# Performance work log

Measured on AMD Instinct MI355X. Metric: run time of the kernel, lower is better.

Reference implementation:

```python
import jax, jax.numpy as jnp
import numpy as np

N_NODES = 50000
N_EDGES = 800000
IN_F = 64
HID_F = 64
OUT_F = 12


def setup_inputs() -> dict:
    key = jax.random.key(0)
    ks = jax.random.split(key, 8)
    x = jax.random.normal(ks[0], (N_NODES, IN_F), dtype=jnp.float32)
    edge_index = jax.random.randint(ks[1], (2, N_EDGES), 0, N_NODES, dtype=jnp.int64)
    edge_attr = jax.random.uniform(ks[2], (N_EDGES, 1), dtype=jnp.float32)
    # Glorot-ish scaled weights
    W1 = jax.random.normal(ks[3], (IN_F, HID_F), dtype=jnp.float32) / np.sqrt(IN_F)
    b1 = jnp.zeros((HID_F,), dtype=jnp.float32)
    W2 = jax.random.normal(ks[4], (HID_F, HID_F), dtype=jnp.float32) / np.sqrt(HID_F)
    b2 = jnp.zeros((HID_F,), dtype=jnp.float32)
    Wfc = jax.random.normal(ks[5], (HID_F, OUT_F), dtype=jnp.float32) / np.sqrt(HID_F)
    bfc = jnp.zeros((OUT_F,), dtype=jnp.float32)
    return {"x": x, "edge_index": edge_index, "edge_attr": edge_attr,
            "W1": W1, "b1": b1, "W2": W2, "b2": b2, "Wfc": Wfc, "bfc": bfc}


def _gcn_conv(h, src, dst, ew, W, b, n_nodes):
    """PyG GCNConv: linear -> add self-loops (weight 1) -> sym-normalized scatter-add -> +bias."""
    hl = h @ W  # [N, F_out]
    loop = jnp.arange(n_nodes, dtype=src.dtype)
    s = jnp.concatenate([src, loop])
    d = jnp.concatenate([dst, loop])
    w = jnp.concatenate([ew, jnp.ones((n_nodes,), dtype=hl.dtype)])
    deg = jax.ops.segment_sum(w, d, num_segments=n_nodes)
    dinv = jnp.where(deg > 0, jax.lax.rsqrt(jnp.maximum(deg, 1e-30)), 0.0)
    norm = dinv[s] * w * dinv[d]  # per-edge coefficient
    out = jax.ops.segment_sum(norm[:, None] * hl[s], d, num_segments=n_nodes)
    return out + b


def reference(x, edge_index, edge_attr, W1, b1, W2, b2, Wfc, bfc):
    src, dst = edge_index[0], edge_index[1]
    ew = edge_attr.squeeze(-1)
    n = x.shape[0]
    h = jax.nn.relu(_gcn_conv(x, src, dst, ew, W1, b1, n))
    h = jax.nn.relu(_gcn_conv(h, src, dst, ew, W2, b2, n))
    return h @ Wfc + bfc
```

## Files before the change

kernel.cpp:

```cpp
#include <hip/hip_runtime.h>
#include <hip/hip_bf16.h>
#include <hip/hip_fp16.h>


#define N_FEAT   64
#define OUT_F    12
#define NTHREADS 256
#define MAXDEG   52
#define AGG_BLOCKS 1792
#define CNT_SHIFT 25
#define SUM_MASK  0x1FFFFFFu
#define FIXS     524288.0f
#define FIXINV   (1.0f / 524288.0f)

struct Params {
    const float* x; const int* idx; const float* ew;
    const float* W1; const float* b1; const float* W2; const float* b2;
    const float* Wfc; const float* bfc;
    float* out;
    int n_nodes, n_edges;
    unsigned int* deg32;
    float* dinv;
    unsigned int* ell;
    __hip_bfloat16* xbf;
    __hip_bfloat16* h1bf;
};

__device__ __forceinline__ float unpack_w(unsigned int e) {
    return __half2float(__ushort_as_half((unsigned short)(e & 0xffffu)));
}

__device__ __forceinline__ void lds_fence() {
    asm volatile("s_waitcnt lgkmcnt(0)" ::: "memory");
}

__device__ __forceinline__ float ell_gather(const __hip_bfloat16* __restrict__ hl,
                                            const unsigned int* __restrict__ row,
                                            int cnt, int lane, float acc) {
    const int nq = cnt >> 2;
    if (nq > 0) {
        uint4 a = *(const uint4*)(row);
        float va0 = __bfloat162float(hl[(a.x >> 16) * 64 + lane]);
        float va1 = __bfloat162float(hl[(a.y >> 16) * 64 + lane]);
        float va2 = __bfloat162float(hl[(a.z >> 16) * 64 + lane]);
        float va3 = __bfloat162float(hl[(a.w >> 16) * 64 + lane]);
        uint4 b = (nq > 1) ? *(const uint4*)(row + 4) : a;
        for (int q = 1; q < nq; q++) {
            uint4 c = (q + 1 < nq) ? *(const uint4*)(row + 4 * (q + 1)) : b;
            float vb0 = __bfloat162float(hl[(b.x >> 16) * 64 + lane]);
            float vb1 = __bfloat162float(hl[(b.y >> 16) * 64 + lane]);
            float vb2 = __bfloat162float(hl[(b.z >> 16) * 64 + lane]);
            float vb3 = __bfloat162float(hl[(b.w >> 16) * 64 + lane]);
            acc += unpack_w(a.x) * va0;
            acc += unpack_w(a.y) * va1;
            acc += unpack_w(a.z) * va2;
            acc += unpack_w(a.w) * va3;
            a = b; va0 = vb0; va1 = vb1; va2 = vb2; va3 = vb3;
            b = c;
        }
        acc += unpack_w(a.x) * va0;
        acc += unpack_w(a.y) * va1;
        acc += unpack_w(a.z) * va2;
        acc += unpack_w(a.w) * va3;
    }
    for (int k = nq << 2; k < cnt; k++) {
        unsigned int e = row[k];
        acc += unpack_w(e) * __bfloat162float(hl[(e >> 16) * 64 + lane]);
    }
    return acc;
}


__global__ void kf_count(Params p) {
    int e2 = blockIdx.x * NTHREADS + threadIdx.x;
    int nE2 = p.n_edges >> 1;
    if (e2 < nE2) {
        int2   s2 = ((const int2*)p.idx)[e2];
        int2   d2 = ((const int2*)(p.idx + p.n_edges))[e2];
        float2 w2 = ((const float2*)p.ew)[e2];
        unsigned int o0 =
            atomicAdd(&p.deg32[d2.x], (1u << CNT_SHIFT) | (unsigned int)(w2.x * FIXS));
        unsigned int o1 =
            atomicAdd(&p.deg32[d2.y], (1u << CNT_SHIFT) | (unsigned int)(w2.y * FIXS));
        int sl0 = (int)(o0 >> CNT_SHIFT);
        int sl1 = (int)(o1 >> CNT_SHIFT);
        if (sl0 < MAXDEG)
            p.ell[d2.x * MAXDEG + sl0] = ((unsigned int)s2.x << 16) |
                                         (unsigned int)__half_as_ushort(__float2half(w2.x));
        if (sl1 < MAXDEG)
            p.ell[d2.y * MAXDEG + sl1] = ((unsigned int)s2.y << 16) |
                                         (unsigned int)__half_as_ushort(__float2half(w2.y));
    }
    if (e2 == 0 && (p.n_edges & 1)) {
        int e = p.n_edges - 1;
        int s = p.idx[e], d = p.idx[p.n_edges + e];
        float w = p.ew[e];
        unsigned int o =
            atomicAdd(&p.deg32[d], (1u << CNT_SHIFT) | (unsigned int)(w * FIXS));
        int sl = (int)(o >> CNT_SHIFT);
        if (sl < MAXDEG)
            p.ell[d * MAXDEG + sl] =
                ((unsigned int)s << 16) | (unsigned int)__half_as_ushort(__float2half(w));
    }
}

__global__ void kf_scalex(Params p) {
    int t = threadIdx.x, b = blockIdx.x, nb = gridDim.x;
    int lane = t & 63;
    int wid  = t >> 6;
    for (int node = b * 4 + wid; node < p.n_nodes; node += nb * 4) {
        unsigned int dv = p.deg32[node];
        float di = rsqrtf((float)(dv & SUM_MASK) * FIXINV + 1.0f);
        float xv = p.x[node * 64 + lane];
        p.xbf[node * 64 + lane] = __float2bfloat16(di * xv);
        if (lane == 0) p.dinv[node] = di;
    }
}

__global__ void kf_agg1g1(Params p) {
    __shared__ float Ws[64 * 64];
    __shared__ float hs[4][64];
    int t = threadIdx.x, b = blockIdx.x, nb = gridDim.x;
    {
        const float4* W4 = (const float4*)p.W1;
        float4* Ws4 = (float4*)Ws;
        for (int i = t; i < 1024; i += NTHREADS) Ws4[i] = W4[i];
    }
    __syncthreads();
    int lane = t & 63;
    int wid  = t >> 6;
    float bv = p.b1[lane];
    float* hrow = hs[wid];
    for (int node = b * 4 + wid; node < p.n_nodes; node += nb * 4) {
        float di = p.dinv[node];
        int cnt = (int)(p.deg32[node] >> CNT_SHIFT);
        cnt = (cnt > MAXDEG) ? MAXDEG : cnt;
        float acc = __bfloat162float(p.xbf[node * 64 + lane]);
        acc = ell_gather(p.xbf, p.ell + (long long)node * MAXDEG, cnt, lane, acc);
        hrow[lane] = di * acc;
        lds_fence();
        float o = 0.f;
#pragma unroll
        for (int k4 = 0; k4 < 16; k4++) {
            float4 hv = *(const float4*)&hrow[k4 * 4];
            int kb = k4 << 2;
            o += hv.x * Ws[(kb + 0) * 64 + lane];
            o += hv.y * Ws[(kb + 1) * 64 + lane];
            o += hv.z * Ws[(kb + 2) * 64 + lane];
            o += hv.w * Ws[(kb + 3) * 64 + lane];
        }
        float h1 = fmaxf(o + bv, 0.0f);
        p.h1bf[node * 64 + lane] = __float2bfloat16(di * h1);
        lds_fence();
    }
}

__global__ void kf_agg2fc(Params p) {
    __shared__ float Ws[64 * 64];
    __shared__ float Wf[64 * OUT_F];
    __shared__ float bf[OUT_F];
    __shared__ float hs[4][64];
    int t = threadIdx.x, b = blockIdx.x, nb = gridDim.x;
    {
        const float4* W4 = (const float4*)p.W2;
        float4* Ws4 = (float4*)Ws;
        for (int i = t; i < 1024; i += NTHREADS) Ws4[i] = W4[i];
    }
    for (int i = t; i < 64 * OUT_F; i += NTHREADS) Wf[i] = p.Wfc[i];
    if (t < OUT_F) bf[t] = p.bfc[t];
    __syncthreads();
    int lane = t & 63;
    int wid  = t >> 6;
    float bv = p.b2[lane];
    float* hrow = hs[wid];
    for (int node = b * 4 + wid; node < p.n_nodes; node += nb * 4) {
        float di  = p.dinv[node];
        int   cnt = (int)(p.deg32[node] >> CNT_SHIFT);
        cnt = (cnt > MAXDEG) ? MAXDEG : cnt;
        float acc = __bfloat162float(p.h1bf[node * 64 + lane]);
        acc = ell_gather(p.h1bf, p.ell + (long long)node * MAXDEG, cnt, lane, acc);
        hrow[lane] = di * acc;
        lds_fence();
        float o = 0.f;
#pragma unroll
        for (int k4 = 0; k4 < 16; k4++) {
            float4 hv = *(const float4*)&hrow[k4 * 4];
            int kb = k4 << 2;
            o += hv.x * Ws[(kb + 0) * 64 + lane];
            o += hv.y * Ws[(kb + 1) * 64 + lane];
            o += hv.z * Ws[(kb + 2) * 64 + lane];
            o += hv.w * Ws[(kb + 3) * 64 + lane];
        }
        float h2 = fmaxf(o + bv, 0.0f);
        lds_fence();
        hrow[lane] = h2;
        lds_fence();
        if (lane < OUT_F) {
            float o2 = bf[lane];
#pragma unroll
            for (int k4 = 0; k4 < 16; k4++) {
                float4 hq = *(const float4*)&hrow[k4 * 4];
                int kb = k4 << 2;
                o2 += hq.x * Wf[(kb + 0) * OUT_F + lane];
                o2 += hq.y * Wf[(kb + 1) * OUT_F + lane];
                o2 += hq.z * Wf[(kb + 2) * OUT_F + lane];
                o2 += hq.w * Wf[(kb + 3) * OUT_F + lane];
            }
            p.out[node * OUT_F + lane] = o2;
        }
        lds_fence();
    }
}

extern "C" void kernel_launch(void* const* d_in, const int* in_sizes, int n_in,
                              void* d_out, int out_size, void* d_ws, size_t ws_size,
                              hipStream_t stream) {
    Params p;
    p.x   = (const float*)d_in[0];
    p.idx = (const int*)d_in[1];
    p.ew  = (const float*)d_in[2];
    p.W1  = (const float*)d_in[3];
    p.b1  = (const float*)d_in[4];
    p.W2  = (const float*)d_in[5];
    p.b2  = (const float*)d_in[6];
    p.Wfc = (const float*)d_in[7];
    p.bfc = (const float*)d_in[8];
    p.out = (float*)d_out;
    p.n_nodes = in_sizes[0] / N_FEAT;
    p.n_edges = in_sizes[2];

    float* ws = (float*)d_ws;
    p.deg32 = (unsigned int*)ws;
    p.dinv  = ws + 100032;
    p.ell   = (unsigned int*)(ws + 150048);
    p.xbf   = (__hip_bfloat16*)(ws + 2750048);
    p.h1bf  = (__hip_bfloat16*)(ws + 4350048);

    int gE2 = (p.n_edges / 2 + NTHREADS - 1) / NTHREADS;

    (void)hipMemsetAsync(ws, 0, 50016u * 4u, stream);
    kf_count <<<gE2,        NTHREADS, 0, stream>>>(p);
    kf_scalex<<<AGG_BLOCKS, NTHREADS, 0, stream>>>(p);
    kf_agg1g1<<<AGG_BLOCKS, NTHREADS, 0, stream>>>(p);
    kf_agg2fc<<<AGG_BLOCKS, NTHREADS, 0, stream>>>(p);
}
```

Before: 213.2 us.

## Prefetch next node's metadata and use wave shuffles instead of LDS rows

Both aggregation kernels now software-pipeline the node loop. The next node's degree word, dinv, self feature and first ELL quad are loaded before the current node's gather runs, which hides the latency of those dependent loads. The per-wave LDS staging row and its waitcnt fences are replaced by __shfl broadcasts for the 64x64 and 64x12 matvecs, and the FC stage now runs on all lanes with clamped indices. The aggregation grid also grows from 1792 to 2048 blocks. The cost is higher register pressure from the prefetched state, and the shuffles go through LDS hardware (ds_bpermute) anyway.

After: 431.3 us. 2.02x slower.

```diff
diff --git a/kernel.cpp b/kernel.cpp
--- a/kernel.cpp
+++ b/kernel.cpp
@@ -7,7 +7,7 @@
 #define OUT_F    12
 #define NTHREADS 256
 #define MAXDEG   52
-#define AGG_BLOCKS 1792
+#define AGG_BLOCKS 2048
 #define CNT_SHIFT 25
 #define SUM_MASK  0x1FFFFFFu
 #define FIXS     524288.0f
@@ -30,16 +30,11 @@
     return __half2float(__ushort_as_half((unsigned short)(e & 0xffffu)));
 }
 
-__device__ __forceinline__ void lds_fence() {
-    asm volatile("s_waitcnt lgkmcnt(0)" ::: "memory");
-}
-
-__device__ __forceinline__ float ell_gather(const __hip_bfloat16* __restrict__ hl,
-                                            const unsigned int* __restrict__ row,
-                                            int cnt, int lane, float acc) {
+__device__ __forceinline__ float ell_gather_pre(const __hip_bfloat16* __restrict__ hl,
+                                                const unsigned int* __restrict__ row,
+                                                int cnt, int lane, float acc, uint4 a) {
     const int nq = cnt >> 2;
     if (nq > 0) {
-        uint4 a = *(const uint4*)(row);
         float va0 = __bfloat162float(hl[(a.x >> 16) * 64 + lane]);
         float va1 = __bfloat162float(hl[(a.y >> 16) * 64 + lane]);
         float va2 = __bfloat162float(hl[(a.z >> 16) * 64 + lane]);
@@ -119,7 +114,6 @@
 
 __global__ void kf_agg1g1(Params p) {
     __shared__ float Ws[64 * 64];
-    __shared__ float hs[4][64];
     int t = threadIdx.x, b = blockIdx.x, nb = gridDim.x;
     {
         const float4* W4 = (const float4*)p.W1;
@@ -130,36 +124,52 @@
     int lane = t & 63;
     int wid  = t >> 6;
     float bv = p.b1[lane];
-    float* hrow = hs[wid];
-    for (int node = b * 4 + wid; node < p.n_nodes; node += nb * 4) {
-        float di = p.dinv[node];
-        int cnt = (int)(p.deg32[node] >> CNT_SHIFT);
+    const int stride = nb * 4;
+    int node = b * 4 + wid;
+    if (node >= p.n_nodes) return;
+    unsigned int dv = p.deg32[node];
+    float di = p.dinv[node];
+    float self = __bfloat162float(p.xbf[node * 64 + lane]);
+    const unsigned int* rowp = p.ell + (long long)node * MAXDEG;
+    uint4 q0 = *(const uint4*)rowp;
+    for (;;) {
+        int nnode = node + stride;
+        bool have_next = (nnode < p.n_nodes);
+        unsigned int ndv = 0; float ndi = 0.f, nself = 0.f;
+        const unsigned int* nrowp = rowp; uint4 nq0 = q0;
+        if (have_next) {
+            ndv   = p.deg32[nnode];
+            ndi   = p.dinv[nnode];
+            nself = __bfloat162float(p.xbf[nnode * 64 + lane]);
+            nrowp = p.ell + (long long)nnode * MAXDEG;
+            nq0   = *(const uint4*)nrowp;
+        }
+        int cnt = (int)(dv >> CNT_SHIFT);
         cnt = (cnt > MAXDEG) ? MAXDEG : cnt;
-        float acc = __bfloat162float(p.xbf[node * 64 + lane]);
-        acc = ell_gather(p.xbf, p.ell + (long long)node * MAXDEG, cnt, lane, acc);
-        hrow[lane] = di * acc;
-        lds_fence();
+        float g = di * ell_gather_pre(p.xbf, rowp, cnt, lane, self, q0);
         float o = 0.f;
 #pragma unroll
-        for (int k4 = 0; k4 < 16; k4++) {
-            float4 hv = *(const float4*)&hrow[k4 * 4];
-            int kb = k4 << 2;
-            o += hv.x * Ws[(kb + 0) * 64 + lane];
-            o += hv.y * Ws[(kb + 1) * 64 + lane];
-            o += hv.z * Ws[(kb + 2) * 64 + lane];
-            o += hv.w * Ws[(kb + 3) * 64 + lane];
+        for (int k = 0; k < 64; k += 4) {
+            float g0 = __shfl(g, k + 0, 64);
+            float g1 = __shfl(g, k + 1, 64);
+            float g2 = __shfl(g, k + 2, 64);
+            float g3 = __shfl(g, k + 3, 64);
+            o += g0 * Ws[(k + 0) * 64 + lane];
+            o += g1 * Ws[(k + 1) * 64 + lane];
+            o += g2 * Ws[(k + 2) * 64 + lane];
+            o += g3 * Ws[(k + 3) * 64 + lane];
         }
         float h1 = fmaxf(o + bv, 0.0f);
         p.h1bf[node * 64 + lane] = __float2bfloat16(di * h1);
-        lds_fence();
+        if (!have_next) break;
+        node = nnode; dv = ndv; di = ndi; self = nself; rowp = nrowp; q0 = nq0;
     }
 }
 
 __global__ void kf_agg2fc(Params p) {
     __shared__ float Ws[64 * 64];
     __shared__ float Wf[64 * OUT_F];
-    __shared__ float bf[OUT_F];
-    __shared__ float hs[4][64];
+    __shared__ float bfs[OUT_F];
     int t = threadIdx.x, b = blockIdx.x, nb = gridDim.x;
     {
         const float4* W4 = (const float4*)p.W2;
@@ -167,48 +177,63 @@
         for (int i = t; i < 1024; i += NTHREADS) Ws4[i] = W4[i];
     }
     for (int i = t; i < 64 * OUT_F; i += NTHREADS) Wf[i] = p.Wfc[i];
-    if (t < OUT_F) bf[t] = p.bfc[t];
+    if (t < OUT_F) bfs[t] = p.bfc[t];
     __syncthreads();
     int lane = t & 63;
     int wid  = t >> 6;
     float bv = p.b2[lane];
-    float* hrow = hs[wid];
-    for (int node = b * 4 + wid; node < p.n_nodes; node += nb * 4) {
-        float di  = p.dinv[node];
-        int   cnt = (int)(p.deg32[node] >> CNT_SHIFT);
+    int lf = (lane < OUT_F) ? lane : 0;
+    const int stride = nb * 4;
+    int node = b * 4 + wid;
+    if (node >= p.n_nodes) return;
+    unsigned int dv = p.deg32[node];
+    float di = p.dinv[node];
+    float self = __bfloat162float(p.h1bf[node * 64 + lane]);
+    const unsigned int* rowp = p.ell + (long long)node * MAXDEG;
+    uint4 q0 = *(const uint4*)rowp;
+    for (;;) {
+        int nnode = node + stride;
+        bool have_next = (nnode < p.n_nodes);
+        unsigned int ndv = 0; float ndi = 0.f, nself = 0.f;
+        const unsigned int* nrowp = rowp; uint4 nq0 = q0;
+        if (have_next) {
+            ndv   = p.deg32[nnode];
+            ndi   = p.dinv[nnode];
+            nself = __bfloat162float(p.h1bf[nnode * 64 + lane]);
+            nrowp = p.ell + (long long)nnode * MAXDEG;
+            nq0   = *(const uint4*)nrowp;
+        }
+        int cnt = (int)(dv >> CNT_SHIFT);
         cnt = (cnt > MAXDEG) ? MAXDEG : cnt;
-        float acc = __bfloat162float(p.h1bf[node * 64 + lane]);
-        acc = ell_gather(p.h1bf, p.ell + (long long)node * MAXDEG, cnt, lane, acc);
-        hrow[lane] = di * acc;
-        lds_fence();
+        float g = di * ell_gather_pre(p.h1bf, rowp, cnt, lane, self, q0);
         float o = 0.f;
 #pragma unroll
-        for (int k4 = 0; k4 < 16; k4++) {
-            float4 hv = *(const float4*)&hrow[k4 * 4];
-            int kb = k4 << 2;
-            o += hv.x * Ws[(kb + 0) * 64 + lane];
-            o += hv.y * Ws[(kb + 1) * 64 + lane];
-            o += hv.z * Ws[(kb + 2) * 64 + lane];
-            o += hv.w * Ws[(kb + 3) * 64 + lane];
+        for (int k = 0; k < 64; k += 4) {
+            float g0 = __shfl(g, k + 0, 64);
+            float g1 = __shfl(g, k + 1, 64);
+            float g2 = __shfl(g, k + 2, 64);
+            float g3 = __shfl(g, k + 3, 64);
+            o += g0 * Ws[(k + 0) * 64 + lane];
+            o += g1 * Ws[(k + 1) * 64 + lane];
+            o += g2 * Ws[(k + 2) * 64 + lane];
+            o += g3 * Ws[(k + 3) * 64 + lane];
         }
         float h2 = fmaxf(o + bv, 0.0f);
-        lds_fence();
-        hrow[lane] = h2;
-        lds_fence();
-        if (lane < OUT_F) {
-            float o2 = bf[lane];
+        float o2 = bfs[lf];
 #pragma unroll
-            for (int k4 = 0; k4 < 16; k4++) {
-                float4 hq = *(const float4*)&hrow[k4 * 4];
-                int kb = k4 << 2;
-                o2 += hq.x * Wf[(kb + 0) * OUT_F + lane];
-                o2 += hq.y * Wf[(kb + 1) * OUT_F + lane];
-                o2 += hq.z * Wf[(kb + 2) * OUT_F + lane];
-                o2 += hq.w * Wf[(kb + 3) * OUT_F + lane];
-            }
-            p.out[node * OUT_F + lane] = o2;
-        }
-        lds_fence();
+        for (int k = 0; k < 64; k += 4) {
+            float h0 = __shfl(h2, k + 0, 64);
+            float h1v = __shfl(h2, k + 1, 64);
+            float h2v = __shfl(h2, k + 2, 64);
+            float h3 = __shfl(h2, k + 3, 64);
+            o2 += h0  * Wf[(k + 0) * OUT_F + lf];
+            o2 += h1v * Wf[(k + 1) * OUT_F + lf];
+            o2 += h2v * Wf[(k + 2) * OUT_F + lf];
+            o2 += h3  * Wf[(k + 3) * OUT_F + lf];
+        }
+        if (lane < OUT_F) p.out[node * OUT_F + lane] = o2;
+        if (!have_next) break;
+        node = nnode; dv = ndv; di = ndi; self = nself; rowp = nrowp; q0 = nq0;
     }
 }
 
```
